# Kernel tuning notes

Hardware: AMD Instinct MI355X
Metric: run time of the kernel (lower is better)

## Reference

```python
import jax, jax.numpy as jnp
import numpy as np
from jax import lax

H = 512      # hidden_dim
P = 11       # num_patches
T = 200      # patch_size
STRIDE = 180 # patch_stride
L = 2000     # output_length
C = 8        # num_target_channels
B = 1024


def _conv1d(x, w, b, pad):
    # x: (B, Cin, L), w: (Cout, Cin, K) torch OIH layout
    y = lax.conv_general_dilated(x, w, window_strides=(1,), padding=[(pad, pad)],
                                 dimension_numbers=('NCH', 'OIH', 'NCH'))
    return y + b[None, :, None]


def _window():
    fade = min(T // 4, 50)
    w = jnp.ones((T,), dtype=jnp.float32)
    ramp = jnp.linspace(0.0, 1.0, fade, dtype=jnp.float32)
    w = w.at[:fade].set(ramp)
    w = w.at[T - fade:].set(ramp[::-1])
    return w


def setup_inputs() -> dict:
    key = jax.random.key(0)
    ks = jax.random.split(key, 16)
    s = 0.02
    return {
        'expanded_embeddings': jax.random.normal(ks[0], (B, P, C, H), dtype=jnp.float32),
        # patch_decoder: Linear(H,H) -> GELU -> (Dropout eval=identity) -> Linear(H,T)
        'W1': jax.random.normal(ks[1], (H, H), dtype=jnp.float32) * s,
        'b1': jnp.zeros((H,), dtype=jnp.float32),
        'W2': jax.random.normal(ks[2], (H, T), dtype=jnp.float32) * s,
        'b2': jnp.zeros((T,), dtype=jnp.float32),
        # refinement: Conv1d(C,4C,15,p7) GELU Conv1d(4C,2C,15,p7) GELU Conv1d(2C,C,15,p7)
        'rw1': jax.random.normal(ks[3], (4 * C, C, 15), dtype=jnp.float32) * s,
        'rb1': jnp.zeros((4 * C,), dtype=jnp.float32),
        'rw2': jax.random.normal(ks[4], (2 * C, 4 * C, 15), dtype=jnp.float32) * s,
        'rb2': jnp.zeros((2 * C,), dtype=jnp.float32),
        'rw3': jax.random.normal(ks[5], (C, 2 * C, 15), dtype=jnp.float32) * s,
        'rb3': jnp.zeros((C,), dtype=jnp.float32),
        # output_proj: Conv1d(C,C,1)
        'pw': jax.random.normal(ks[6], (C, C, 1), dtype=jnp.float32) * s,
        'pb': jnp.zeros((C,), dtype=jnp.float32),
    }


def reference(expanded_embeddings, W1, b1, W2, b2, rw1, rb1, rw2, rb2, rw3, rb3, pw, pb):
    gelu = lambda x: jax.nn.gelu(x, approximate=False)  # torch default GELU (erf)
    # per-patch MLP decode: (B,P,C,H) -> (B,P,C,T)
    h = gelu(jnp.einsum('bpch,hd->bpcd', expanded_embeddings, W1) + b1)
    patches = jnp.einsum('bpch,ht->bpct', h, W2) + b2

    # overlap-add with triangular-faded window
    win = _window()  # (T,)
    out = jnp.zeros((B, C, L), dtype=jnp.float32)
    wsum = jnp.zeros((L,), dtype=jnp.float32)  # identical across B,C
    for i in range(P):  # small static loop over patches
        s0 = i * STRIDE
        if s0 + T <= L:
            out = out.at[:, :, s0:s0 + T].add(patches[:, i] * win)
            wsum = wsum.at[s0:s0 + T].add(win)
    rec = out / jnp.clip(wsum, 1e-8)[None, None, :]

    # conv refinement + residual
    r = gelu(_conv1d(rec, rw1, rb1, 7))
    r = gelu(_conv1d(r, rw2, rb2, 7))
    r = _conv1d(r, rw3, rb3, 7)
    rec = rec + r
    return _conv1d(rec, pw, pb, 0)
```

## Files before the change

kernel.cpp:

```cpp
#include <hip/hip_runtime.h>
#include <stdint.h>
#include <stddef.h>

#define HD 512
#define NP 11
#define PT 200
#define PSTRIDE 180
#define OL 2000
#define NC 8
#define NB 1024

typedef __bf16 bf16x8 __attribute__((ext_vector_type(8)));
typedef float floatx4 __attribute__((ext_vector_type(4)));

__device__ __forceinline__ unsigned short f2bf(float f) {
    unsigned int u = __float_as_uint(f);
    u = u + 0x7FFFu + ((u >> 16) & 1u);
    return (unsigned short)(u >> 16);
}
__device__ __forceinline__ float gelu_erf(float x) {
    return 0.5f * x * (1.0f + erff(x * 0.70710678118654752440f));
}

__global__ __launch_bounds__(256) void cast_x_kernel(const float* __restrict__ x,
                                                     unsigned short* __restrict__ xb) {
    int idx = blockIdx.x * 256 + threadIdx.x;
    float4 v = ((const float4*)x)[idx];
    ushort4 o;
    o.x = f2bf(v.x); o.y = f2bf(v.y); o.z = f2bf(v.z); o.w = f2bf(v.w);
    ((ushort4*)xb)[idx] = o;
}

__global__ __launch_bounds__(256) void prep_w_kernel(const float* __restrict__ W1,
                                                     const float* __restrict__ W2,
                                                     unsigned short* __restrict__ W1t,
                                                     unsigned short* __restrict__ W2t) {
    int idx = blockIdx.x * 256 + threadIdx.x;
    if (idx < 512 * 512) {
        int n = idx >> 9, k = idx & 511;
        W1t[idx] = f2bf(W1[k * 512 + n]);
    } else {
        int j = idx - 512 * 512;
        int n = j >> 9, k = j & 511;
        W2t[j] = (n < PT) ? f2bf(W2[k * PT + n]) : (unsigned short)0;
    }
}

__global__ __launch_bounds__(256) void prep_cw_kernel(const float* __restrict__ rw1,
                                                      const float* __restrict__ rw2,
                                                      const float* __restrict__ rw3,
                                                      unsigned short* __restrict__ Wt1,
                                                      unsigned short* __restrict__ Wt2,
                                                      unsigned short* __restrict__ Wt3) {
    int idx = blockIdx.x * 256 + threadIdx.x;
    if (idx < 4096) {
        int kb = idx >> 10, rem = idx & 1023, oc = rem >> 5, k = rem & 31;
        int tl = k >> 3, ic = k & 7, tap = kb * 4 + tl;
        Wt1[idx] = (tap < 15) ? f2bf(rw1[(oc * 8 + ic) * 15 + tap]) : (unsigned short)0;
    } else if (idx < 4096 + 7680) {
        int j = idx - 4096;
        int t = j >> 9, rem = j & 511, oc = rem >> 5, ic = rem & 31;
        Wt2[j] = f2bf(rw2[(oc * 32 + ic) * 15 + t]);
    } else {
        int j = idx - 11776;
        int kb = j >> 9, rem = j & 511, m = rem >> 5, k = rem & 31;
        int tl = k >> 4, ic = k & 15, tap = kb * 2 + tl;
        Wt3[j] = (m < 8 && tap < 15) ? f2bf(rw3[(m * 16 + ic) * 15 + tap]) : (unsigned short)0;
    }
}

template<bool FUSE_GELU, bool OUT_BF16>
__global__ __launch_bounds__(256) void gemm_kernel(const unsigned short* __restrict__ A,
                                                   const unsigned short* __restrict__ Bt,
                                                   const float* __restrict__ bias,
                                                   void* __restrict__ Cout,
                                                   int out_stride, int n_valid) {
    __shared__ __align__(16) unsigned short As[128 * 32];
    __shared__ __align__(16) unsigned short Bs[128 * 32];
    const int tid  = threadIdx.x;
    const int lane = tid & 63;
    const int wid  = tid >> 6;
    const int m0 = blockIdx.x * 128;
    const int n0 = blockIdx.y * 128;
    const int mw = (wid >> 1) * 64;
    const int nw = (wid & 1) * 64;
    const int l15  = lane & 15;
    const int quad = lane >> 4;

    floatx4 acc[4][4];
#pragma unroll
    for (int i = 0; i < 4; ++i)
#pragma unroll
        for (int j = 0; j < 4; ++j) acc[i][j] = (floatx4)0.0f;

    for (int k0 = 0; k0 < 512; k0 += 32) {
#pragma unroll
        for (int p = 0; p < 2; ++p) {
            int ci  = tid + p * 256;
            int row = ci >> 2;
            int c16 = ci & 3;
            int4 va = *(const int4*)(A  + (size_t)(m0 + row) * 512 + k0 + c16 * 8);
            *(int4*)(As + row * 32 + c16 * 8) = va;
            int4 vb = *(const int4*)(Bt + (size_t)(n0 + row) * 512 + k0 + c16 * 8);
            *(int4*)(Bs + row * 32 + c16 * 8) = vb;
        }
        __syncthreads();
        bf16x8 af[4], bfr[4];
#pragma unroll
        for (int t = 0; t < 4; ++t) {
            af[t]  = *(const bf16x8*)(As + (mw + t * 16 + l15) * 32 + quad * 8);
            bfr[t] = *(const bf16x8*)(Bs + (nw + t * 16 + l15) * 32 + quad * 8);
        }
#pragma unroll
        for (int mt = 0; mt < 4; ++mt)
#pragma unroll
            for (int nt = 0; nt < 4; ++nt)
                acc[mt][nt] = __builtin_amdgcn_mfma_f32_16x16x32_bf16(af[mt], bfr[nt], acc[mt][nt], 0, 0, 0);
        __syncthreads();
    }

#pragma unroll
    for (int mt = 0; mt < 4; ++mt) {
#pragma unroll
        for (int nt = 0; nt < 4; ++nt) {
            const int col  = n0 + nw + nt * 16 + l15;
            const int rowb = m0 + mw + mt * 16 + quad * 4;
            const bool colok = (col < n_valid);
            float bv = colok ? bias[col] : 0.0f;
#pragma unroll
            for (int r = 0; r < 4; ++r) {
                float v = acc[mt][nt][r] + bv;
                if (FUSE_GELU) v = gelu_erf(v);
                if (colok) {
                    size_t off = (size_t)(rowb + r) * out_stride + col;
                    if (OUT_BF16) ((unsigned short*)Cout)[off] = f2bf(v);
                    else          ((float*)Cout)[off] = v;
                }
            }
        }
    }
}

__global__ __launch_bounds__(256) void oadd_kernel(const float* __restrict__ patches,
                                                   float* __restrict__ rec) {
    int idx = blockIdx.x * 256 + threadIdx.x;
    int l = idx % OL;
    int b = idx / OL;
    int imin = (l >= PT) ? (l - (PT - PSTRIDE)) / PSTRIDE : 0;
    int imax = l / PSTRIDE; if (imax > NP - 1) imax = NP - 1;
    float acc[8];
#pragma unroll
    for (int c = 0; c < 8; ++c) acc[c] = 0.0f;
    float wsum = 0.0f;
    for (int i = imin; i <= imax; ++i) {
        int t = l - i * PSTRIDE;
        float w = (t < 50) ? t * (1.0f / 49.0f)
                           : ((t >= 150) ? (199 - t) * (1.0f / 49.0f) : 1.0f);
        wsum += w;
        const float* p = patches + ((size_t)(b * NP + i) * NC) * PT + t;
#pragma unroll
        for (int c = 0; c < 8; ++c) acc[c] += p[c * PT] * w;
    }
    float inv = 1.0f / fmaxf(wsum, 1e-8f);
    float4 v0 = { acc[0] * inv, acc[1] * inv, acc[2] * inv, acc[3] * inv };
    float4 v1 = { acc[4] * inv, acc[5] * inv, acc[6] * inv, acc[7] * inv };
    float* o = rec + (size_t)idx * 8;
    *(float4*)o = v0;
    *(float4*)(o + 4) = v1;
}

__global__ __launch_bounds__(256) void conv1_mfma(const float* __restrict__ rec,
                                                  const unsigned short* __restrict__ Wt1,
                                                  const float* __restrict__ rb1,
                                                  unsigned short* __restrict__ c1) {
    __shared__ __align__(16) unsigned short xs[272 * 8];
    __shared__ __align__(16) unsigned short ys[256 * 40];
    __shared__ float bs[32];
    const int tid = threadIdx.x;
    const int b = blockIdx.y;
    const int seg0 = blockIdx.x * 256;
    const int lane = tid & 63, wid = tid >> 6;
    const int l15 = lane & 15, quad = lane >> 4;

    if (tid < 32) bs[tid] = rb1[tid];
    for (int i = tid; i < 544; i += 256) {
        int row = i >> 1, half = i & 1;
        int p = seg0 - 7 + row;
        float4 v = (p >= 0 && p < OL) ? *(const float4*)(rec + ((size_t)b * OL + p) * 8 + half * 4)
                                      : make_float4(0.f, 0.f, 0.f, 0.f);
        ushort4 o; o.x = f2bf(v.x); o.y = f2bf(v.y); o.z = f2bf(v.z); o.w = f2bf(v.w);
        *(ushort4*)(xs + row * 8 + half * 4) = o;
    }
    bf16x8 wfrag[4][2];
#pragma unroll
    for (int kb = 0; kb < 4; ++kb)
#pragma unroll
        for (int ot = 0; ot < 2; ++ot)
            wfrag[kb][ot] = *(const bf16x8*)(Wt1 + (kb * 32 + ot * 16 + l15) * 32 + quad * 8);
    __syncthreads();

    floatx4 acc[2][4];
#pragma unroll
    for (int ot = 0; ot < 2; ++ot)
#pragma unroll
        for (int u = 0; u < 4; ++u) acc[ot][u] = (floatx4)0.0f;

#pragma unroll
    for (int u = 0; u < 4; ++u) {
        const int posl = wid * 64 + u * 16 + l15;
#pragma unroll
        for (int kb = 0; kb < 4; ++kb) {
            int row = posl + kb * 4 + quad;
            bf16x8 bfrag = *(const bf16x8*)(xs + row * 8);
#pragma unroll
            for (int ot = 0; ot < 2; ++ot)
                acc[ot][u] = __builtin_amdgcn_mfma_f32_16x16x32_bf16(wfrag[kb][ot], bfrag, acc[ot][u], 0, 0, 0);
        }
    }
#pragma unroll
    for (int ot = 0; ot < 2; ++ot)
#pragma unroll
        for (int u = 0; u < 4; ++u) {
            int posl = wid * 64 + u * 16 + l15;
#pragma unroll
            for (int r = 0; r < 4; ++r) {
                int oc = ot * 16 + quad * 4 + r;
                ys[posl * 40 + oc] = f2bf(gelu_erf(acc[ot][u][r] + bs[oc]));
            }
        }
    __syncthreads();
    for (int i = tid; i < 1024; i += 256) {
        int row = i >> 2, ch = i & 3;
        int p = seg0 + row;
        if (p < OL)
            *(int4*)(c1 + ((size_t)b * OL + p) * 32 + ch * 8) = *(const int4*)(ys + row * 40 + ch * 8);
    }
}

__global__ __launch_bounds__(256) void conv2_mfma(const unsigned short* __restrict__ c1,
                                                  const unsigned short* __restrict__ Wt2,
                                                  const float* __restrict__ rb2,
                                                  unsigned short* __restrict__ c2) {
    __shared__ __align__(16) unsigned short xs[270 * 40];
    __shared__ __align__(16) unsigned short ys[256 * 24];
    __shared__ float bs[16];
    const int tid = threadIdx.x;
    const int b = blockIdx.y;
    const int seg0 = blockIdx.x * 256;
    const int lane = tid & 63, wid = tid >> 6;
    const int l15 = lane & 15, quad = lane >> 4;

    if (tid < 16) bs[tid] = rb2[tid];
    for (int i = tid; i < 1080; i += 256) {
        int row = i >> 2, ch = i & 3;
        int p = seg0 - 7 + row;
        int4 v = (p >= 0 && p < OL) ? *(const int4*)(c1 + ((size_t)b * OL + p) * 32 + ch * 8)
                                    : make_int4(0, 0, 0, 0);
        *(int4*)(xs + row * 40 + ch * 8) = v;
    }
    bf16x8 wfrag[15];
#pragma unroll
    for (int t = 0; t < 15; ++t)
        wfrag[t] = *(const bf16x8*)(Wt2 + (t * 16 + l15) * 32 + quad * 8);
    __syncthreads();

    floatx4 acc[4];
#pragma unroll
    for (int u = 0; u < 4; ++u) acc[u] = (floatx4)0.0f;

#pragma unroll
    for (int u = 0; u < 4; ++u) {
        const int posl = wid * 64 + u * 16 + l15;
#pragma unroll
        for (int t = 0; t < 15; ++t) {
            bf16x8 bfrag = *(const bf16x8*)(xs + (posl + t) * 40 + quad * 8);
            acc[u] = __builtin_amdgcn_mfma_f32_16x16x32_bf16(wfrag[t], bfrag, acc[u], 0, 0, 0);
        }
    }
#pragma unroll
    for (int u = 0; u < 4; ++u) {
        int posl = wid * 64 + u * 16 + l15;
#pragma unroll
        for (int r = 0; r < 4; ++r) {
            int oc = quad * 4 + r;
            ys[posl * 24 + oc] = f2bf(gelu_erf(acc[u][r] + bs[oc]));
        }
    }
    __syncthreads();
    for (int i = tid; i < 512; i += 256) {
        int row = i >> 1, ch = i & 1;
        int p = seg0 + row;
        if (p < OL)
            *(int4*)(c2 + ((size_t)b * OL + p) * 16 + ch * 8) = *(const int4*)(ys + row * 24 + ch * 8);
    }
}

__global__ __launch_bounds__(256) void conv3pw_mfma(const unsigned short* __restrict__ c2,
                                                    const float* __restrict__ rec,
                                                    const unsigned short* __restrict__ Wt3,
                                                    const float* __restrict__ rb3,
                                                    const float* __restrict__ pw,
                                                    const float* __restrict__ pb,
                                                    float* __restrict__ out) {
    __shared__ __align__(16) unsigned short xs[272 * 24];
    __shared__ __align__(16) float r2[256 * 12];
    __shared__ float pws[64], bs3[8], bsp[8];
    const int tid = threadIdx.x;
    const int b = blockIdx.y;
    const int seg0 = blockIdx.x * 256;
    const int lane = tid & 63, wid = tid >> 6;
    const int l15 = lane & 15, quad = lane >> 4;

    if (tid < 64) pws[tid] = pw[tid];
    if (tid >= 64 && tid < 72) bs3[tid - 64] = rb3[tid - 64];
    if (tid >= 72 && tid < 80) bsp[tid - 72] = pb[tid - 72];
    for (int i = tid; i < 544; i += 256) {
        int row = i >> 1, ch = i & 1;
        int p = seg0 - 7 + row;
        int4 v = (p >= 0 && p < OL) ? *(const int4*)(c2 + ((size_t)b * OL + p) * 16 + ch * 8)
                                    : make_int4(0, 0, 0, 0);
        *(int4*)(xs + row * 24 + ch * 8) = v;
    }
    for (int i = tid; i < 512; i += 256) {
        int row = i >> 1, half = i & 1;
        int p = seg0 + row;
        float4 v = (p < OL) ? *(const float4*)(rec + ((size_t)b * OL + p) * 8 + half * 4)
                            : make_float4(0.f, 0.f, 0.f, 0.f);
        *(float4*)(r2 + row * 12 + half * 4) = v;
    }
    bf16x8 wfrag[8];
#pragma unroll
    for (int kb = 0; kb < 8; ++kb)
        wfrag[kb] = *(const bf16x8*)(Wt3 + (kb * 16 + l15) * 32 + quad * 8);
    __syncthreads();

    floatx4 acc[4];
#pragma unroll
    for (int u = 0; u < 4; ++u) acc[u] = (floatx4)0.0f;

#pragma unroll
    for (int u = 0; u < 4; ++u) {
        const int posl = wid * 64 + u * 16 + l15;
#pragma unroll
        for (int kb = 0; kb < 8; ++kb) {
            int row = posl + kb * 2 + (quad >> 1);
            bf16x8 bfrag = *(const bf16x8*)(xs + row * 24 + (quad & 1) * 8);
            acc[u] = __builtin_amdgcn_mfma_f32_16x16x32_bf16(wfrag[kb], bfrag, acc[u], 0, 0, 0);
        }
    }
    if (quad < 2) {
#pragma unroll
        for (int u = 0; u < 4; ++u) {
            int posl = wid * 64 + u * 16 + l15;
#pragma unroll
            for (int r = 0; r < 4; ++r) {
                int oc = quad * 4 + r;
                r2[posl * 12 + oc] += acc[u][r] + bs3[oc];
            }
        }
    }
    __syncthreads();
    {
        int p = seg0 + tid;
        if (p < OL) {
            float4 a = *(const float4*)(r2 + tid * 12);
            float4 c = *(const float4*)(r2 + tid * 12 + 4);
#pragma unroll
            for (int o = 0; o < 8; ++o) {
                float v = bsp[o];
                v += pws[o * 8 + 0] * a.x + pws[o * 8 + 1] * a.y + pws[o * 8 + 2] * a.z + pws[o * 8 + 3] * a.w;
                v += pws[o * 8 + 4] * c.x + pws[o * 8 + 5] * c.y + pws[o * 8 + 6] * c.z + pws[o * 8 + 7] * c.w;
                out[((size_t)b * 8 + o) * OL + p] = v;
            }
        }
    }
}

extern "C" void kernel_launch(void* const* d_in, const int* in_sizes, int n_in,
                              void* d_out, int out_size, void* d_ws, size_t ws_size,
                              hipStream_t stream) {
    const float* X   = (const float*)d_in[0];
    const float* W1  = (const float*)d_in[1];
    const float* b1  = (const float*)d_in[2];
    const float* W2  = (const float*)d_in[3];
    const float* b2  = (const float*)d_in[4];
    const float* rw1 = (const float*)d_in[5];
    const float* rb1 = (const float*)d_in[6];
    const float* rw2 = (const float*)d_in[7];
    const float* rb2 = (const float*)d_in[8];
    const float* rw3 = (const float*)d_in[9];
    const float* rb3 = (const float*)d_in[10];
    const float* pw  = (const float*)d_in[11];
    const float* pb  = (const float*)d_in[12];
    float* out = (float*)d_out;

    char* ws = (char*)d_ws;
    unsigned short* Xb  = (unsigned short*)(ws);
    unsigned short* W1t = (unsigned short*)(ws +  92274688);
    unsigned short* W2t = (unsigned short*)(ws +  92798976);
    unsigned short* h   = (unsigned short*)(ws +  93061120);
    float*          pat = (float*)         (ws + 185335808);
    float*          rec = (float*)         (ws + 257425408);
    unsigned short* Wt1 = (unsigned short*)(ws + 322961408);
    unsigned short* Wt2 = (unsigned short*)(ws + 322969600);
    unsigned short* Wt3 = (unsigned short*)(ws + 322984960);
    unsigned short* c1  = (unsigned short*)(ws);
    unsigned short* c2  = (unsigned short*)(ws + 131072000);

    cast_x_kernel<<<45056, 256, 0, stream>>>(X, Xb);
    prep_w_kernel<<<1536, 256, 0, stream>>>(W1, W2, W1t, W2t);
    prep_cw_kernel<<<62, 256, 0, stream>>>(rw1, rw2, rw3, Wt1, Wt2, Wt3);
    gemm_kernel<true,  true ><<<dim3(704, 4), 256, 0, stream>>>(Xb, W1t, b1, (void*)h,   512, 512);
    gemm_kernel<false, false><<<dim3(704, 2), 256, 0, stream>>>(h,  W2t, b2, (void*)pat, 200, 200);
    oadd_kernel<<<8000, 256, 0, stream>>>(pat, rec);
    conv1_mfma<<<dim3(8, NB), 256, 0, stream>>>(rec, Wt1, rb1, c1);
    conv2_mfma<<<dim3(8, NB), 256, 0, stream>>>(c1, Wt2, rb2, c2);
    conv3pw_mfma<<<dim3(8, NB), 256, 0, stream>>>(c2, rec, Wt3, rb3, pw, pb, out);
}
```

Before: 651.4 us.

## Use direct global-to-LDS loads in GEMMs, bf16 patches, swizzled tiles, vector epilogues

The GEMM tile staging now uses global_load_lds to copy A and B tiles straight into shared memory instead of going through registers. Block indices are remapped into 1D groups of 8 M-tiles per N-tile to improve L2 reuse. The second GEMM writes patches in bf16, halving that intermediate's traffic, and the overlap-add reads them back as bf16. The conv epilogues pack their four outputs into vectorized LDS stores. Rounding patches to bf16 adds precision loss on the decoded patches.

```diff
diff --git a/kernel.cpp b/kernel.cpp
--- a/kernel.cpp
+++ b/kernel.cpp
@@ -18,8 +18,16 @@
     u = u + 0x7FFFu + ((u >> 16) & 1u);
     return (unsigned short)(u >> 16);
 }
+__device__ __forceinline__ float bf2f(unsigned short s) {
+    return __uint_as_float(((unsigned int)s) << 16);
+}
 __device__ __forceinline__ float gelu_erf(float x) {
     return 0.5f * x * (1.0f + erff(x * 0.70710678118654752440f));
+}
+__device__ __forceinline__ void async16(const unsigned short* g, unsigned short* l) {
+    __builtin_amdgcn_global_load_lds(
+        (const __attribute__((address_space(1))) unsigned int*)g,
+        (__attribute__((address_space(3))) unsigned int*)l, 16, 0, 0);
 }
 
 __global__ __launch_bounds__(256) void cast_x_kernel(const float* __restrict__ x,
@@ -69,23 +77,28 @@
     }
 }
 
-template<bool FUSE_GELU, bool OUT_BF16>
-__global__ __launch_bounds__(256) void gemm_kernel(const unsigned short* __restrict__ A,
-                                                   const unsigned short* __restrict__ Bt,
-                                                   const float* __restrict__ bias,
-                                                   void* __restrict__ Cout,
-                                                   int out_stride, int n_valid) {
+template<bool FUSE_GELU, bool OUT_BF16, int LOG2_NT>
+__global__ __launch_bounds__(256) void gemm_lds_kernel(const unsigned short* __restrict__ A,
+                                                       const unsigned short* __restrict__ Bt,
+                                                       const float* __restrict__ bias,
+                                                       void* __restrict__ Cout,
+                                                       int out_stride, int n_valid) {
     __shared__ __align__(16) unsigned short As[128 * 32];
     __shared__ __align__(16) unsigned short Bs[128 * 32];
     const int tid  = threadIdx.x;
     const int lane = tid & 63;
     const int wid  = tid >> 6;
-    const int m0 = blockIdx.x * 128;
-    const int n0 = blockIdx.y * 128;
+    const int bid  = blockIdx.x;
+    const int nt   = (bid >> 3) & ((1 << LOG2_NT) - 1);
+    const int mt   = (bid >> (3 + LOG2_NT)) * 8 + (bid & 7);
+    const int m0 = mt * 128;
+    const int n0 = nt * 128;
     const int mw = (wid >> 1) * 64;
     const int nw = (wid & 1) * 64;
     const int l15  = lane & 15;
     const int quad = lane >> 4;
+    const int srow = lane >> 2;
+    const int scol = (lane & 3) * 8;
 
     floatx4 acc[4][4];
 #pragma unroll
@@ -96,13 +109,9 @@
     for (int k0 = 0; k0 < 512; k0 += 32) {
 #pragma unroll
         for (int p = 0; p < 2; ++p) {
-            int ci  = tid + p * 256;
-            int row = ci >> 2;
-            int c16 = ci & 3;
-            int4 va = *(const int4*)(A  + (size_t)(m0 + row) * 512 + k0 + c16 * 8);
-            *(int4*)(As + row * 32 + c16 * 8) = va;
-            int4 vb = *(const int4*)(Bt + (size_t)(n0 + row) * 512 + k0 + c16 * 8);
-            *(int4*)(Bs + row * 32 + c16 * 8) = vb;
+            const int rbase = wid * 32 + p * 16;
+            async16(A  + (size_t)(m0 + rbase + srow) * 512 + k0 + scol, As + rbase * 32);
+            async16(Bt + (size_t)(n0 + rbase + srow) * 512 + k0 + scol, Bs + rbase * 32);
         }
         __syncthreads();
         bf16x8 af[4], bfr[4];
@@ -112,24 +121,24 @@
             bfr[t] = *(const bf16x8*)(Bs + (nw + t * 16 + l15) * 32 + quad * 8);
         }
 #pragma unroll
-        for (int mt = 0; mt < 4; ++mt)
-#pragma unroll
-            for (int nt = 0; nt < 4; ++nt)
-                acc[mt][nt] = __builtin_amdgcn_mfma_f32_16x16x32_bf16(af[mt], bfr[nt], acc[mt][nt], 0, 0, 0);
+        for (int mtl = 0; mtl < 4; ++mtl)
+#pragma unroll
+            for (int ntl = 0; ntl < 4; ++ntl)
+                acc[mtl][ntl] = __builtin_amdgcn_mfma_f32_16x16x32_bf16(af[mtl], bfr[ntl], acc[mtl][ntl], 0, 0, 0);
         __syncthreads();
     }
 
 #pragma unroll
-    for (int mt = 0; mt < 4; ++mt) {
-#pragma unroll
-        for (int nt = 0; nt < 4; ++nt) {
-            const int col  = n0 + nw + nt * 16 + l15;
-            const int rowb = m0 + mw + mt * 16 + quad * 4;
+    for (int mtl = 0; mtl < 4; ++mtl) {
+#pragma unroll
+        for (int ntl = 0; ntl < 4; ++ntl) {
+            const int col  = n0 + nw + ntl * 16 + l15;
+            const int rowb = m0 + mw + mtl * 16 + quad * 4;
             const bool colok = (col < n_valid);
             float bv = colok ? bias[col] : 0.0f;
 #pragma unroll
             for (int r = 0; r < 4; ++r) {
-                float v = acc[mt][nt][r] + bv;
+                float v = acc[mtl][ntl][r] + bv;
                 if (FUSE_GELU) v = gelu_erf(v);
                 if (colok) {
                     size_t off = (size_t)(rowb + r) * out_stride + col;
@@ -141,7 +150,7 @@
     }
 }
 
-__global__ __launch_bounds__(256) void oadd_kernel(const float* __restrict__ patches,
+__global__ __launch_bounds__(256) void oadd_kernel(const unsigned short* __restrict__ patches,
                                                    float* __restrict__ rec) {
     int idx = blockIdx.x * 256 + threadIdx.x;
     int l = idx % OL;
@@ -157,9 +166,9 @@
         float w = (t < 50) ? t * (1.0f / 49.0f)
                            : ((t >= 150) ? (199 - t) * (1.0f / 49.0f) : 1.0f);
         wsum += w;
-        const float* p = patches + ((size_t)(b * NP + i) * NC) * PT + t;
-#pragma unroll
-        for (int c = 0; c < 8; ++c) acc[c] += p[c * PT] * w;
+        const unsigned short* p = patches + ((size_t)(b * NP + i) * NC) * PT + t;
+#pragma unroll
+        for (int c = 0; c < 8; ++c) acc[c] += bf2f(p[c * PT]) * w;
     }
     float inv = 1.0f / fmaxf(wsum, 1e-8f);
     float4 v0 = { acc[0] * inv, acc[1] * inv, acc[2] * inv, acc[3] * inv };
@@ -222,11 +231,13 @@
 #pragma unroll
         for (int u = 0; u < 4; ++u) {
             int posl = wid * 64 + u * 16 + l15;
-#pragma unroll
-            for (int r = 0; r < 4; ++r) {
-                int oc = ot * 16 + quad * 4 + r;
-                ys[posl * 40 + oc] = f2bf(gelu_erf(acc[ot][u][r] + bs[oc]));
-            }
+            int oc0 = ot * 16 + quad * 4;
+            ushort4 o;
+            o.x = f2bf(gelu_erf(acc[ot][u][0] + bs[oc0]));
+            o.y = f2bf(gelu_erf(acc[ot][u][1] + bs[oc0 + 1]));
+            o.z = f2bf(gelu_erf(acc[ot][u][2] + bs[oc0 + 2]));
+            o.w = f2bf(gelu_erf(acc[ot][u][3] + bs[oc0 + 3]));
+            *(ushort4*)(ys + posl * 40 + oc0) = o;
         }
     __syncthreads();
     for (int i = tid; i < 1024; i += 256) {
@@ -280,11 +291,13 @@
 #pragma unroll
     for (int u = 0; u < 4; ++u) {
         int posl = wid * 64 + u * 16 + l15;
-#pragma unroll
-        for (int r = 0; r < 4; ++r) {
-            int oc = quad * 4 + r;
-            ys[posl * 24 + oc] = f2bf(gelu_erf(acc[u][r] + bs[oc]));
-        }
+        int oc0 = quad * 4;
+        ushort4 o;
+        o.x = f2bf(gelu_erf(acc[u][0] + bs[oc0]));
+        o.y = f2bf(gelu_erf(acc[u][1] + bs[oc0 + 1]));
+        o.z = f2bf(gelu_erf(acc[u][2] + bs[oc0 + 2]));
+        o.w = f2bf(gelu_erf(acc[u][3] + bs[oc0 + 3]));
+        *(ushort4*)(ys + posl * 24 + oc0) = o;
     }
     __syncthreads();
     for (int i = tid; i < 512; i += 256) {
@@ -352,11 +365,13 @@
 #pragma unroll
         for (int u = 0; u < 4; ++u) {
             int posl = wid * 64 + u * 16 + l15;
-#pragma unroll
-            for (int r = 0; r < 4; ++r) {
-                int oc = quad * 4 + r;
-                r2[posl * 12 + oc] += acc[u][r] + bs3[oc];
-            }
+            int oc0 = quad * 4;
+            float4 rv = *(const float4*)(r2 + posl * 12 + oc0);
+            rv.x += acc[u][0] + bs3[oc0];
+            rv.y += acc[u][1] + bs3[oc0 + 1];
+            rv.z += acc[u][2] + bs3[oc0 + 2];
+            rv.w += acc[u][3] + bs3[oc0 + 3];
+            *(float4*)(r2 + posl * 12 + oc0) = rv;
         }
     }
     __syncthreads();
@@ -399,7 +414,7 @@
     unsigned short* W1t = (unsigned short*)(ws +  92274688);
     unsigned short* W2t = (unsigned short*)(ws +  92798976);
     unsigned short* h   = (unsigned short*)(ws +  93061120);
-    float*          pat = (float*)         (ws + 185335808);
+    unsigned short* pat = (unsigned short*)(ws + 185335808);
     float*          rec = (float*)         (ws + 257425408);
     unsigned short* Wt1 = (unsigned short*)(ws + 322961408);
     unsigned short* Wt2 = (unsigned short*)(ws + 322969600);
@@ -410,8 +425,8 @@
     cast_x_kernel<<<45056, 256, 0, stream>>>(X, Xb);
     prep_w_kernel<<<1536, 256, 0, stream>>>(W1, W2, W1t, W2t);
     prep_cw_kernel<<<62, 256, 0, stream>>>(rw1, rw2, rw3, Wt1, Wt2, Wt3);
-    gemm_kernel<true,  true ><<<dim3(704, 4), 256, 0, stream>>>(Xb, W1t, b1, (void*)h,   512, 512);
-    gemm_kernel<false, false><<<dim3(704, 2), 256, 0, stream>>>(h,  W2t, b2, (void*)pat, 200, 200);
+    gemm_lds_kernel<true,  true, 2><<<2816, 256, 0, stream>>>(Xb, W1t, b1, (void*)h,   512, 512);
+    gemm_lds_kernel<false, true, 1><<<1408, 256, 0, stream>>>(h,  W2t, b2, (void*)pat, 200, 200);
     oadd_kernel<<<8000, 256, 0, stream>>>(pat, rec);
     conv1_mfma<<<dim3(8, NB), 256, 0, stream>>>(rec, Wt1, rb1, c1);
     conv2_mfma<<<dim3(8, NB), 256, 0, stream>>>(c1, Wt2, rb2, c2);
```

Result: faster. 602.6 us (-7.5%).
